# Optimization experiments

Hardware: AMD Instinct MI355X
Metric: run time of the kernel (lower is better)

Reference implementation:

```python
import jax, jax.numpy as jnp
import numpy as np

E = 256
CH = 16  # channel rows; features viewed as (16,16)


def _sigmoid_np(x):
    return 1.0 / (1.0 + np.exp(-x))


def _schedule(emb, comp_l, comp_r, cb, seqs):
    """Phase 1 (host/numpy, mirrors the detached torch control flow):
    runs the iterative argmax-merge tree construction and records the
    integer merge schedule (new composed node pairs per iteration) and the
    (target, ctx_left, ctx_right) prediction triples. Matches Banyan.compose."""
    emb = np.asarray(emb, np.float32)
    sl = _sigmoid_np(np.asarray(comp_l, np.float32))
    sr = _sigmoid_np(np.asarray(comp_r, np.float32))
    cbn = np.asarray(cb, np.float32)
    seqs = np.asarray(seqs, np.int64)

    uniq = np.unique(seqs)
    lookup = np.zeros(uniq.max() + 1, np.int64)
    lookup[uniq] = np.arange(len(uniq))
    lookup[uniq[-1]] = -1  # max unique value acts as pad sentinel (lookup[-1] = -1)
    index = lookup[seqs].copy()
    tokens = uniq[:-1]

    nodes = emb[tokens]  # detached node features used only for similarity / schedule

    def comp(f):  # f: (K,2,16,16)
        return (f[:, 0] * sl + f[:, 1] * sr + cbn).reshape(f.shape[0], -1)

    pair_src = np.zeros((0, 2), np.int64)
    pair_dst = np.zeros((0,), np.int64)
    new_pairs, targets = [], []
    B, W = index.shape

    while W != 1:
        valid = index != -1
        f = nodes[np.clip(index, 0, None)]              # (B,W,E)
        a, b = f[:, :-1], f[:, 1:]
        na = np.linalg.norm(a, axis=-1)
        nb = np.linalg.norm(b, axis=-1)
        cos = (a * b).sum(-1) / np.maximum(na * nb, 1e-8)
        cos = np.where(valid[:, 1:], cos, -np.inf)       # right slot padded -> -inf
        ms_all = np.argmax(cos, axis=1)
        active = ~np.all(index[:, 1:] == -1, axis=1)
        rows = np.nonzero(active)[0]
        ms = ms_all[rows]
        lp, rp = ms, ms + 1
        src = np.stack([index[rows, lp], index[rows, rp]], 1)  # (A,2)

        # dedup against existing composed pairs, then unique new pairs (sorted)
        if pair_src.shape[0] > 0 and src.shape[0] > 0:
            exists = (src[:, None, :] == pair_src[None]).all(-1).any(1)
            newp = src[~exists]
        else:
            newp = src
        if newp.shape[0] > 0:
            newp = np.unique(newp, axis=0)
        base = nodes.shape[0]
        if newp.shape[0] > 0:
            nodes = np.concatenate([nodes, comp(nodes[newp].reshape(-1, 2, CH, CH))], 0)
            pair_src = np.concatenate([pair_src, newp], 0)
            pair_dst = np.concatenate([pair_dst, base + np.arange(newp.shape[0])], 0)
        new_pairs.append(newp.astype(np.int64))

        # neighbourhood targets (get_neighbours): l_t block then r_t block
        lefts, rights = src[:, 0], src[:, 1]
        ls = index[rows, lp - 1].copy()
        ls[lp - 1 == -1] = -1
        rs = index[rows, np.minimum(rp + 1, W - 1)].copy()
        rs[rp + 1 == W] = -2
        targets.append(np.stack([lefts, ls, rights], 1))
        targets.append(np.stack([rights, lefts, rs], 1))

        # point both merged slots at the (possibly shared) composed node id
        if src.shape[0] > 0:
            eq = (src[:, None, :] == pair_src[None]).all(-1)
            nid = pair_dst[eq.argmax(1)]
            index[rows, lp] = nid
            index[rows, rp] = nid

        # reduce frontier: active rows drop the left merge slot, inactive drop last col
        keep = np.ones_like(index, dtype=bool)
        keep[rows, ms] = False
        keep[~active, -1] = False
        index = index[keep].reshape(B, W - 1)
        W -= 1

    targets = np.concatenate(targets, 0).astype(np.int64)
    return tokens, new_pairs, targets


def _replay(emb, comp_l, comp_r, cb, sos, eos, tokens, new_pairs, targets):
    """Phase 2 (jax, differentiable): rebuild node features following the
    recorded schedule, then compute the context->target cross entropy."""
    sl = jax.nn.sigmoid(comp_l)
    sr = jax.nn.sigmoid(comp_r)
    feats = emb[tokens]                                    # (n_tok, E)
    for p in new_pairs:
        if p.shape[0] == 0:
            continue
        f = feats[p].reshape(-1, 2, CH, CH)                # (K,2,16,16)
        feats = jnp.concatenate([feats, (f[:, 0] * sl + f[:, 1] * sr + cb).reshape(-1, E)], 0)
    feats = jnp.concatenate([feats, eos[None, :], sos[None, :]], 0)
    N = feats.shape[0]
    t = np.where(targets < 0, targets + N, targets)        # wrap -1 -> sos, -2 -> eos
    l = feats[t[:, 1]].reshape(-1, CH, CH)
    r = feats[t[:, 2]].reshape(-1, CH, CH)
    outs = (l * sl + r * sr + cb).reshape(-1, E)           # (T,E)
    logits = outs @ feats.T                                # (T,N)
    logp = jax.nn.log_softmax(logits, axis=-1)
    return -jnp.mean(logp[jnp.arange(t.shape[0]), t[:, 0]])


def setup_inputs() -> dict:
    key = jax.random.key(0)
    k1, k2, k3, k4, k5, k6, k7 = jax.random.split(key, 7)
    V, B, L = 30000, 64, 64
    tok = jax.random.randint(k1, (B, L), 0, V - 1, dtype=jnp.int32)
    lengths = jax.random.randint(k2, (B,), L // 2, L + 1, dtype=jnp.int32)
    lengths = lengths.at[0].set(L // 2)  # guarantee pad token (V-1) is present
    x = jnp.where(jnp.arange(L)[None, :] < lengths[:, None], tok, V - 1)
    return {
        "x": x,
        "emb": jax.random.normal(k3, (V, E), jnp.float32),
        "comp_l": jax.random.uniform(k4, (CH,), jnp.float32, 0.6, 0.9),
        "comp_r": jax.random.uniform(k5, (CH,), jnp.float32, 0.6, 0.9),
        "cb": jnp.zeros((CH,), jnp.float32),
        "sos": 0.02 * jax.random.normal(k6, (E,), jnp.float32),
        "eos": 0.02 * jax.random.normal(k7, (E,), jnp.float32),
    }


def reference(x, emb, comp_l, comp_r, cb, sos, eos):
    tokens, new_pairs, targets = _schedule(emb, comp_l, comp_r, cb, x)
    return _replay(emb, comp_l, comp_r, cb, sos, eos, tokens, new_pairs, targets)
```

## Files before the change

### kernel.cpp

```cpp
#include <hip/hip_runtime.h>
#include <math.h>


#define NMAX 8192
#define PRES 30720
#define HBITS 13
#define HSIZE 8192
#define HMASK 8191
#define LOG2E 1.44269504f
#define LN2 0.69314718f

typedef float f32x4 __attribute__((ext_vector_type(4)));
typedef short short8 __attribute__((ext_vector_type(8)));

__device__ __forceinline__ unsigned hash0(int key) {
    return (((unsigned)key) * 2654435761u) >> (32 - HBITS);
}

__device__ __forceinline__ unsigned short f2bf(float f) {
    unsigned u = __float_as_uint(f);
    unsigned r = ((u >> 16) & 1u) + 0x7FFFu;
    return (unsigned short)((u + r) >> 16);
}

__device__ __forceinline__ float rdl_f(float v, int lane) {
    return __int_as_float(__builtin_amdgcn_readlane(__float_as_int(v), lane));
}

#define SUM_STEP(CTRL, X) \
    X += __int_as_float(__builtin_amdgcn_update_dpp(0, __float_as_int(X), CTRL, 0xF, 0xF, true));
#define SUM3_REDUCE(A, B, C) {                                                  \
    SUM_STEP(0x121, A) SUM_STEP(0x121, B) SUM_STEP(0x121, C)                    \
    SUM_STEP(0x122, A) SUM_STEP(0x122, B) SUM_STEP(0x122, C)                    \
    SUM_STEP(0x124, A) SUM_STEP(0x124, B) SUM_STEP(0x124, C)                    \
    SUM_STEP(0x128, A) SUM_STEP(0x128, B) SUM_STEP(0x128, C)                    \
    A = rdl_f(A, 0) + rdl_f(A, 16) + rdl_f(A, 32) + rdl_f(A, 48);               \
    B = rdl_f(B, 0) + rdl_f(B, 16) + rdl_f(B, 32) + rdl_f(B, 48);               \
    C = rdl_f(C, 0) + rdl_f(C, 16) + rdl_f(C, 32) + rdl_f(C, 48);               \
}
#define ARGMAX_STEP(CTRL, V, I) {                                               \
    float _ov = __int_as_float(__builtin_amdgcn_update_dpp(0, __float_as_int(V), CTRL, 0xF, 0xF, true)); \
    int _oi = __builtin_amdgcn_update_dpp(0, I, CTRL, 0xF, 0xF, true);          \
    if (_ov > V || (_ov == V && _oi < I)) { V = _ov; I = _oi; }                 \
}
#define ARGMAX_REDUCE(V, I) {                                                   \
    ARGMAX_STEP(0x121, V, I) ARGMAX_STEP(0x122, V, I)                           \
    ARGMAX_STEP(0x124, V, I) ARGMAX_STEP(0x128, V, I)                           \
    float _v0 = rdl_f(V, 0), _v1 = rdl_f(V, 16), _v2 = rdl_f(V, 32), _v3 = rdl_f(V, 48); \
    int _i0 = __builtin_amdgcn_readlane(I, 0), _i1 = __builtin_amdgcn_readlane(I, 16);   \
    int _i2 = __builtin_amdgcn_readlane(I, 32), _i3 = __builtin_amdgcn_readlane(I, 48);  \
    V = _v0; I = _i0;                                                           \
    if (_v1 > V || (_v1 == V && _i1 < I)) { V = _v1; I = _i1; }                 \
    if (_v2 > V || (_v2 == V && _i2 < I)) { V = _v2; I = _i2; }                 \
    if (_v3 > V || (_v3 == V && _i3 < I)) { V = _v3; I = _i3; }                 \
}

__global__ __launch_bounds__(1024) void prep_kernel(
    const int* __restrict__ x, int* __restrict__ tokens,
    int* __restrict__ meta, int* __restrict__ index_g) {
    __shared__ int pres[PRES];
    __shared__ int part[1024];
    int tid = threadIdx.x;
    for (int i = tid; i < PRES; i += 1024) pres[i] = 0;
    __syncthreads();
    for (int i = tid; i < 4096; i += 1024) pres[x[i]] = 1;
    __syncthreads();
    int base = tid * 30;
    int loc[30];
    int s = 0;
#pragma unroll
    for (int i = 0; i < 30; ++i) { loc[i] = s; s += pres[base + i]; }
    part[tid] = s;
    __syncthreads();
    for (int off = 1; off < 1024; off <<= 1) {
        int v = (tid >= off) ? part[tid - off] : 0;
        __syncthreads();
        part[tid] += v;
        __syncthreads();
    }
    int excl = (tid == 0) ? 0 : part[tid - 1];
    int total = part[1023];
#pragma unroll
    for (int i = 0; i < 30; ++i) {
        if (pres[base + i]) tokens[excl + loc[i]] = base + i;
    }
    if (tid == 0) { meta[0] = total; meta[1] = total - 1; }
    __syncthreads();
#pragma unroll
    for (int i = 0; i < 30; ++i) pres[base + i] = excl + loc[i];
    __syncthreads();
    for (int i = tid; i < 4096; i += 1024) {
        int r = pres[x[i]];
        index_g[i] = (r == total - 1) ? -1 : r;
    }
}

__global__ void copy_feats_kernel(const float* __restrict__ emb, const int* __restrict__ tokens,
                                  const int* __restrict__ meta, float* __restrict__ feats,
                                  float* __restrict__ norms) {
    int n = blockIdx.x;
    if (n >= meta[1]) return;
    int t = tokens[n];
    int k = threadIdx.x;
    const float4* src = (const float4*)(emb + (size_t)t * 256);
    float4* dst = (float4*)(feats + (size_t)n * 256);
    float4 v = src[k];
    dst[k] = v;
    float ss = v.x * v.x + v.y * v.y + v.z * v.z + v.w * v.w;
#pragma unroll
    for (int off = 32; off >= 1; off >>= 1) ss += __shfl_down(ss, off);
    if (k == 0) norms[n] = sqrtf(ss);
}

__global__ void init_cos_kernel(const float* __restrict__ feats, const float* __restrict__ norms,
                                const int* __restrict__ index_g, float* __restrict__ cos_g) {
    int bid = blockIdx.x;
    int b = bid / 63, j = bid % 63;
    int l = index_g[b * 64 + j], r = index_g[b * 64 + j + 1];
    float c = -INFINITY;
    if (r != -1) {
        int k = threadIdx.x;
        const float4* fa = (const float4*)(feats + (size_t)l * 256);
        const float4* fb = (const float4*)(feats + (size_t)r * 256);
        float4 a = fa[k], bb = fb[k];
        float d = a.x * bb.x + a.y * bb.y + a.z * bb.z + a.w * bb.w;
#pragma unroll
        for (int off = 32; off >= 1; off >>= 1) d += __shfl_down(d, off);
        c = d / fmaxf(norms[l] * norms[r], 1e-8f);
    }
    if (threadIdx.x == 0) cos_g[b * 64 + j] = c;
}


__global__ __launch_bounds__(64) void treebuild_kernel(
    const float* __restrict__ feats, const float* __restrict__ norms_g,
    const int* __restrict__ index_g, const float* __restrict__ cos_g,
    float* __restrict__ rowfeats, int4* __restrict__ rec,
    const float* __restrict__ comp_l, const float* __restrict__ comp_r,
    const float* __restrict__ cb) {
    __shared__ float lf[127][256];
    __shared__ int4 s_rec[63];
    int b = blockIdx.x;
    int lane = threadIdx.x;
    int c0 = 4 * (lane & 3);
    float4 sl4 = make_float4(1.f / (1.f + __expf(-comp_l[c0])),
                             1.f / (1.f + __expf(-comp_l[c0 + 1])),
                             1.f / (1.f + __expf(-comp_l[c0 + 2])),
                             1.f / (1.f + __expf(-comp_l[c0 + 3])));
    float4 sr4 = make_float4(1.f / (1.f + __expf(-comp_r[c0])),
                             1.f / (1.f + __expf(-comp_r[c0 + 1])),
                             1.f / (1.f + __expf(-comp_r[c0 + 2])),
                             1.f / (1.f + __expf(-comp_r[c0 + 3])));
    float4 cb4 = make_float4(cb[c0], cb[c0 + 1], cb[c0 + 2], cb[c0 + 3]);

    int gid = index_g[b * 64 + lane];
    int isreal = (gid >= 0) ? 1 : 0;
    for (int j = 0; j < 64; ++j) {
        int g = index_g[b * 64 + j];
        int gc = g < 0 ? 0 : g;
        ((float4*)&lf[j][0])[lane] = ((const float4*)(feats + (size_t)gc * 256))[lane];
    }
    float n0 = (gid >= 0) ? norms_g[gid] : 0.f;
    float n1 = 0.f;
    float cosr = (lane < 63) ? cos_g[b * 64 + lane] : -INFINITY;
    int locid = lane;
    unsigned long long alive = ~0ull;
    int nreal = 64 - __popcll(__ballot(gid < 0));

    float Mv = cosr; int Mi = lane;
    ARGMAX_REDUCE(Mv, Mi);

    for (int it = 0; it < 63; ++it) {
        int act = (nreal >= 2) ? 1 : 0;
        int p = Mi;
        unsigned long long after = (alive >> 1) >> p;
        int q = (p + 1 + __builtin_ctzll(after | 0x8000000000000000ull)) & 63;
        unsigned long long bel = alive & ((1ull << p) - 1ull);
        int pp = bel ? (63 - __builtin_clzll(bel)) : -1;
        unsigned long long aft2 = (q < 63) ? (alive >> (q + 1)) : 0ull;
        int ssp = aft2 ? (q + 1 + __builtin_ctzll(aft2)) : -1;
        int l_loc = __builtin_amdgcn_readlane(locid, p);
        int r_loc = __builtin_amdgcn_readlane(locid, q);
        int lsl = __builtin_amdgcn_readlane(locid, pp < 0 ? 0 : pp);
        int rsl = __builtin_amdgcn_readlane(locid, ssp < 0 ? 0 : ssp);
        int ls_loc = (pp >= 0) ? lsl : -1;
        int rs_loc = (ssp >= 0) ? rsl : -2;
        int Creal = (ssp >= 0) ? __builtin_amdgcn_readlane(isreal, ssp) : 0;
        if (lane == 0)
            s_rec[it] = make_int4(act ? l_loc : -9, r_loc, ls_loc, rs_loc);
        if (act) {
            float4 a = ((const float4*)&lf[l_loc][0])[lane];
            float4 bb = ((const float4*)&lf[r_loc][0])[lane];
            float4 av = (pp >= 0) ? ((const float4*)&lf[ls_loc < 0 ? 0 : ls_loc][0])[lane]
                                  : make_float4(0.f, 0.f, 0.f, 0.f);
            float4 cv = Creal ? ((const float4*)&lf[rs_loc < 0 ? 0 : rs_loc][0])[lane]
                              : make_float4(0.f, 0.f, 0.f, 0.f);
            float mv = (lane == p || lane == q || lane == pp) ? -INFINITY : cosr;
            float Mv2 = mv; int Mi2 = lane;
            ARGMAX_REDUCE(Mv2, Mi2);
            int nl = 64 + it;
            float4 v;
            v.x = a.x * sl4.x + bb.x * sr4.x + cb4.x;
            v.y = a.y * sl4.y + bb.y * sr4.y + cb4.y;
            v.z = a.z * sl4.z + bb.z * sr4.z + cb4.z;
            v.w = a.w * sl4.w + bb.w * sr4.w + cb4.w;
            ((float4*)&lf[nl][0])[lane] = v;
            float sv = v.x * v.x + v.y * v.y + v.z * v.z + v.w * v.w;
            float da = av.x * v.x + av.y * v.y + av.z * v.z + av.w * v.w;
            float dc = cv.x * v.x + cv.y * v.y + cv.z * v.z + cv.w * v.w;
            SUM3_REDUCE(sv, da, dc);
            float nn = sqrtf(sv);
            if (lane == it) n1 = nn;
            float nA = 1.f, nC = 1.f;
            if (pp >= 0) nA = (ls_loc < 64) ? rdl_f(n0, ls_loc) : rdl_f(n1, ls_loc - 64);
            if (Creal)   nC = (rs_loc < 64) ? rdl_f(n0, rs_loc) : rdl_f(n1, rs_loc - 64);
            float cosA = da * __builtin_amdgcn_rcpf(fmaxf(nA * nn, 1e-8f));
            float cosC = Creal ? (dc * __builtin_amdgcn_rcpf(fmaxf(nn * nC, 1e-8f))) : -INFINITY;
            if (lane == p) { cosr = cosC; locid = nl; }
            if (lane == pp) cosr = cosA;
            if (lane == q) cosr = -INFINITY;
            if (pp >= 0 && (cosA > Mv2 || (cosA == Mv2 && pp < Mi2))) { Mv2 = cosA; Mi2 = pp; }
            if (cosC > Mv2 || (cosC == Mv2 && p < Mi2)) { Mv2 = cosC; Mi2 = p; }
            Mv = Mv2; Mi = Mi2;
            alive &= ~(1ull << q);
            nreal -= 1;
        }
    }
    for (int it = 0; it < 63; ++it) {
        ((float4*)(rowfeats + ((size_t)b * 63 + it) * 256))[lane] =
            ((const float4*)&lf[64 + it][0])[lane];
    }
    if (lane < 63) rec[b * 63 + lane] = s_rec[lane];
}


__global__ __launch_bounds__(64) void idassign_kernel(
    const int4* __restrict__ rec, const int* __restrict__ index_g,
    int* __restrict__ targets, int* __restrict__ meta, int* __restrict__ newsrc) {
    __shared__ int s_map[64][128];
    __shared__ int s_hk[HSIZE], s_hv[HSIZE];
    int b = threadIdx.x;
    for (int i = b; i < HSIZE; i += 64) s_hk[i] = -1;
    for (int i = b; i < 4096; i += 64) s_map[i >> 6][i & 63] = index_g[i];
    int N0 = meta[1];
    int Ncur = N0, Tcur = 0;
    __syncthreads();
    int4 R = rec[b * 63];
    for (int it = 0; it < 63; ++it) {
        int4 Rn = R;
        if (it + 1 < 63) Rn = rec[b * 63 + it + 1];
        int act = (R.x != -9) ? 1 : 0;
        int l_g = 0, r_g = 0, key = 0, nid = 0;
        int ls_g = -1, rs_g = -2;
        unsigned h = 0;
        int won = 0, need = 0;
        if (act) {
            l_g = s_map[b][R.x];
            r_g = s_map[b][R.y];
            ls_g = (R.z >= 0) ? s_map[b][R.z] : R.z;
            rs_g = (R.w >= 0) ? s_map[b][R.w] : R.w;
            key = (l_g << HBITS) | r_g;
            h = hash0(key);
            need = 1;
        }
        while (__any(need)) {
            if (need) {
                int prev = atomicCAS(&s_hk[h], -1, key);
                if (prev == -1) { won = 1; need = 0; }
                else if (prev == key) { need = 0; }
                else { h = (h + 1) & HMASK; }
            }
        }
        unsigned long long actmask = __ballot(act != 0);
        unsigned long long winmask = __ballot(won != 0);
        unsigned long long below = (1ull << b) - 1ull;
        int ar = __popcll(actmask & below);
        int nact = __popcll(actmask);
        int newc = __popcll(winmask);
        if (won) {
            nid = Ncur + __popcll(winmask & below);
            s_hv[h] = nid;
        }
        __syncthreads();
        if (act && !won) nid = s_hv[h];
        if (won) newsrc[nid - N0] = (b << 6) | it;
        if (act) {
            int o1 = Tcur + ar;
            targets[o1 * 3 + 0] = l_g;
            targets[o1 * 3 + 1] = ls_g;
            targets[o1 * 3 + 2] = r_g;
            int o2 = Tcur + nact + ar;
            targets[o2 * 3 + 0] = r_g;
            targets[o2 * 3 + 1] = l_g;
            targets[o2 * 3 + 2] = rs_g;
            s_map[b][64 + it] = nid;
        }
        Ncur += newc;
        Tcur += 2 * nact;
        R = Rn;
    }
    if (b == 0) { meta[2] = Ncur; meta[3] = Tcur; meta[4] = Ncur - N0; }
}


__global__ __launch_bounds__(64) void materialize_kernel(
    const float* __restrict__ rowfeats, const int* __restrict__ newsrc,
    const int* __restrict__ meta, float* __restrict__ feats,
    const float* __restrict__ eos, const float* __restrict__ sos) {
    int g = blockIdx.x;
    int lane = threadIdx.x;
    if (g == 4032) {
        int n = meta[2];
        ((float4*)(feats + (size_t)n * 256))[lane] = ((const float4*)eos)[lane];
        ((float4*)(feats + (size_t)(n + 1) * 256))[lane] = ((const float4*)sos)[lane];
        return;
    }
    if (g >= meta[4]) return;
    int pk = newsrc[g];
    int b = pk >> 6, it = pk & 63;
    int N0 = meta[1];
    ((float4*)(feats + (size_t)(N0 + g) * 256))[lane] =
        ((const float4*)(rowfeats + ((size_t)b * 63 + it) * 256))[lane];
}

__global__ __launch_bounds__(256) void convert_feats_kernel(
    const float* __restrict__ feats, short8* __restrict__ fhT) {
    int g = blockIdx.x * 256 + threadIdx.x;
    int tile = g >> 9, rem = g & 511;
    int ks = rem >> 6, lane64 = rem & 63;
    int kq = lane64 >> 4, col = lane64 & 15;
    int row = tile * 16 + col;
    int e0 = (ks * 4 + kq) * 8;
    const float4* src = (const float4*)(feats + (size_t)row * 256 + e0);
    float4 v0 = src[0], v1 = src[1];
    short8 o;
    o[0] = (short)f2bf(v0.x); o[1] = (short)f2bf(v0.y);
    o[2] = (short)f2bf(v0.z); o[3] = (short)f2bf(v0.w);
    o[4] = (short)f2bf(v1.x); o[5] = (short)f2bf(v1.y);
    o[6] = (short)f2bf(v1.z); o[7] = (short)f2bf(v1.w);
    fhT[g] = o;
}

__global__ __launch_bounds__(256) void prep_outs_kernel(
    const float* __restrict__ feats, const int* __restrict__ targets,
    const int* __restrict__ meta, const float* __restrict__ comp_l,
    const float* __restrict__ comp_r, const float* __restrict__ cb,
    unsigned short* __restrict__ oh, float* __restrict__ tdot) {
    int T = meta[3];
    int Ntot = meta[2] + 2;
    int t = blockIdx.x * 4 + (threadIdx.x >> 6);
    if (t >= T) return;
    int lane = threadIdx.x & 63;
    int c0 = 4 * (lane & 3);
    float4 sl4 = make_float4(1.f / (1.f + __expf(-comp_l[c0])),
                             1.f / (1.f + __expf(-comp_l[c0 + 1])),
                             1.f / (1.f + __expf(-comp_l[c0 + 2])),
                             1.f / (1.f + __expf(-comp_l[c0 + 3])));
    float4 sr4 = make_float4(1.f / (1.f + __expf(-comp_r[c0])),
                             1.f / (1.f + __expf(-comp_r[c0 + 1])),
                             1.f / (1.f + __expf(-comp_r[c0 + 2])),
                             1.f / (1.f + __expf(-comp_r[c0 + 3])));
    float4 cb4 = make_float4(cb[c0], cb[c0 + 1], cb[c0 + 2], cb[c0 + 3]);
    int t0 = targets[t * 3 + 0];
    int i1 = targets[t * 3 + 1], i2 = targets[t * 3 + 2];
    if (i1 < 0) i1 += Ntot;
    if (i2 < 0) i2 += Ntot;
    float4 a = ((const float4*)(feats + (size_t)i1 * 256))[lane];
    float4 b = ((const float4*)(feats + (size_t)i2 * 256))[lane];
    float4 ft = ((const float4*)(feats + (size_t)t0 * 256))[lane];
    float4 v;
    v.x = a.x * sl4.x + b.x * sr4.x + cb4.x;
    v.y = a.y * sl4.y + b.y * sr4.y + cb4.y;
    v.z = a.z * sl4.z + b.z * sr4.z + cb4.z;
    v.w = a.w * sl4.w + b.w * sr4.w + cb4.w;
    float d = v.x * ft.x + v.y * ft.y + v.z * ft.z + v.w * ft.w;
#pragma unroll
    for (int off = 32; off >= 1; off >>= 1) d += __shfl_down(d, off);
    if (lane == 0) tdot[t] = d;
    ushort4 h;
    h.x = f2bf(v.x); h.y = f2bf(v.y); h.z = f2bf(v.z); h.w = f2bf(v.w);
    ((ushort4*)(oh + (size_t)t * 256))[lane] = h;
}

__global__ __launch_bounds__(512) void loss_mfma_kernel(
    const short8* __restrict__ fhT, const unsigned short* __restrict__ oh,
    const int* __restrict__ meta, float2* __restrict__ partial) {
    __shared__ float s_m[64][2], s_s[64][2];
    int T = meta[3];
    int Ntot = meta[2] + 2;
    int row0 = blockIdx.x * 64;
    if (row0 >= T) return;
    int slab = blockIdx.y;
    int P = (Ntot + 127) >> 7;
    int cstart = slab * (P << 5);
    int cend = min(Ntot, cstart + (P << 5));
    int tid = threadIdx.x, lane = tid & 63, w = tid >> 6;
    int mq = w >> 1, nq = w & 1;
    int mrow = row0 + mq * 16 + (lane & 15);
    int kq = lane >> 4;
    const short8* pah = (const short8*)(oh + (size_t)mrow * 256);
    short8 Ah[8];
#pragma unroll
    for (int ks = 0; ks < 8; ++ks) Ah[ks] = pah[ks * 4 + kq];
    float m0 = -1e30f, m1 = -1e30f, m2 = -1e30f, m3 = -1e30f;
    float s0 = 0.f, s1 = 0.f, s2 = 0.f, s3 = 0.f;
    for (int nb = cstart; nb < cend; nb += 32) {
        const short8* pb = fhT + ((size_t)(nb >> 4) + nq) * 512;
        f32x4 a0 = {0.f, 0.f, 0.f, 0.f}, a1 = a0;
#pragma unroll
        for (int ks = 0; ks < 4; ++ks) {
            a0 = __builtin_amdgcn_mfma_f32_16x16x32_bf16(Ah[ks], pb[ks * 64 + lane], a0, 0, 0, 0);
            a1 = __builtin_amdgcn_mfma_f32_16x16x32_bf16(Ah[ks + 4], pb[(ks + 4) * 64 + lane], a1, 0, 0, 0);
        }
        int col = nb + nq * 16 + (lane & 15);
        bool cv = col < cend;
        float v0 = cv ? (a0[0] + a1[0]) * LOG2E : -INFINITY;
        float v1 = cv ? (a0[1] + a1[1]) * LOG2E : -INFINITY;
        float v2 = cv ? (a0[2] + a1[2]) * LOG2E : -INFINITY;
        float v3 = cv ? (a0[3] + a1[3]) * LOG2E : -INFINITY;
        if (v0 > m0) { s0 = s0 * exp2f(m0 - v0) + 1.f; m0 = v0; } else s0 += exp2f(v0 - m0);
        if (v1 > m1) { s1 = s1 * exp2f(m1 - v1) + 1.f; m1 = v1; } else s1 += exp2f(v1 - m1);
        if (v2 > m2) { s2 = s2 * exp2f(m2 - v2) + 1.f; m2 = v2; } else s2 += exp2f(v2 - m2);
        if (v3 > m3) { s3 = s3 * exp2f(m3 - v3) + 1.f; m3 = v3; } else s3 += exp2f(v3 - m3);
    }
#pragma unroll
    for (int off = 1; off < 16; off <<= 1) {
        float mo, so, mn;
        mo = __shfl_xor(m0, off); so = __shfl_xor(s0, off);
        mn = fmaxf(m0, mo); s0 = s0 * exp2f(m0 - mn) + so * exp2f(mo - mn); m0 = mn;
        mo = __shfl_xor(m1, off); so = __shfl_xor(s1, off);
        mn = fmaxf(m1, mo); s1 = s1 * exp2f(m1 - mn) + so * exp2f(mo - mn); m1 = mn;
        mo = __shfl_xor(m2, off); so = __shfl_xor(s2, off);
        mn = fmaxf(m2, mo); s2 = s2 * exp2f(m2 - mn) + so * exp2f(mo - mn); m2 = mn;
        mo = __shfl_xor(m3, off); so = __shfl_xor(s3, off);
        mn = fmaxf(m3, mo); s3 = s3 * exp2f(m3 - mn) + so * exp2f(mo - mn); m3 = mn;
    }
    if ((lane & 15) == 0) {
        int rbase = mq * 16 + kq * 4;
        s_m[rbase + 0][nq] = m0; s_s[rbase + 0][nq] = s0;
        s_m[rbase + 1][nq] = m1; s_s[rbase + 1][nq] = s1;
        s_m[rbase + 2][nq] = m2; s_s[rbase + 2][nq] = s2;
        s_m[rbase + 3][nq] = m3; s_s[rbase + 3][nq] = s3;
    }
    __syncthreads();
    if (tid < 64) {
        float ma = s_m[tid][0], mb = s_m[tid][1];
        float mn = fmaxf(ma, mb);
        float ss = s_s[tid][0] * exp2f(ma - mn) + s_s[tid][1] * exp2f(mb - mn);
        partial[(size_t)slab * NMAX + row0 + tid] = make_float2(mn, ss);
    }
}

__global__ __launch_bounds__(1024) void combine_kernel(
    const float2* __restrict__ partial, const float* __restrict__ tdot,
    const int* __restrict__ meta, float* __restrict__ out) {
    __shared__ float red[16];
    int T = meta[3];
    float loss = 0.f;
    for (int r = threadIdx.x; r < T; r += 1024) {
        float2 p0 = partial[r];
        float2 p1 = partial[NMAX + r];
        float2 p2 = partial[2 * NMAX + r];
        float2 p3 = partial[3 * NMAX + r];
        float mn = fmaxf(fmaxf(p0.x, p1.x), fmaxf(p2.x, p3.x));
        float ss = p0.y * exp2f(p0.x - mn) + p1.y * exp2f(p1.x - mn) +
                   p2.y * exp2f(p2.x - mn) + p3.y * exp2f(p3.x - mn);
        loss += (mn + __log2f(ss)) * LN2 - tdot[r];
    }
#pragma unroll
    for (int off = 32; off >= 1; off >>= 1) loss += __shfl_down(loss, off);
    if ((threadIdx.x & 63) == 0) red[threadIdx.x >> 6] = loss;
    __syncthreads();
    if (threadIdx.x < 16) {
        loss = red[threadIdx.x];
#pragma unroll
        for (int off = 8; off >= 1; off >>= 1) loss += __shfl_down(loss, off);
        if (threadIdx.x == 0) out[0] = loss / (float)T;
    }
}

extern "C" void kernel_launch(void* const* d_in, const int* in_sizes, int n_in,
                              void* d_out, int out_size, void* d_ws, size_t ws_size,
                              hipStream_t stream) {
    const int* x = (const int*)d_in[0];
    const float* emb = (const float*)d_in[1];
    const float* comp_l = (const float*)d_in[2];
    const float* comp_r = (const float*)d_in[3];
    const float* cb = (const float*)d_in[4];
    const float* sos = (const float*)d_in[5];
    const float* eos = (const float*)d_in[6];
    float* out = (float*)d_out;

    float* feats = (float*)d_ws;
    float* norms = feats + (size_t)NMAX * 256;
    int* index_g = (int*)(norms + NMAX);
    float* cos_g = (float*)(index_g + 4096);
    int* tokens = (int*)(cos_g + 4096);
    int* targets = tokens + 4096;
    int* meta = targets + NMAX * 3;
    float* tdot = (float*)(meta + 64);
    float2* partial = (float2*)(tdot + NMAX);
    int4* rec = (int4*)(partial + 4 * NMAX);
    int* newsrc = (int*)(rec + 64 * 63);
    float* rowfeats = (float*)(newsrc + 4096);
    short8* fhT = (short8*)(rowfeats + (size_t)64 * 63 * 256);
    unsigned short* oh = (unsigned short*)(fhT + (size_t)NMAX * 32);

    prep_kernel<<<1, 1024, 0, stream>>>(x, tokens, meta, index_g);
    copy_feats_kernel<<<4096, 64, 0, stream>>>(emb, tokens, meta, feats, norms);
    init_cos_kernel<<<64 * 63, 64, 0, stream>>>(feats, norms, index_g, cos_g);
    treebuild_kernel<<<64, 64, 0, stream>>>(feats, norms, index_g, cos_g,
                                            rowfeats, rec, comp_l, comp_r, cb);
    idassign_kernel<<<1, 64, 0, stream>>>(rec, index_g, targets, meta, newsrc);
    materialize_kernel<<<4033, 64, 0, stream>>>(rowfeats, newsrc, meta, feats, eos, sos);
    convert_feats_kernel<<<1024, 256, 0, stream>>>(feats, fhT);
    prep_outs_kernel<<<2016, 256, 0, stream>>>(feats, targets, meta, comp_l, comp_r,
                                               cb, oh, tdot);
    loss_mfma_kernel<<<dim3(126, 4), 512, 0, stream>>>(fhT, oh, meta, partial);
    combine_kernel<<<1, 1024, 0, stream>>>(partial, tdot, meta, out);
}
```

Before: 214.1 us.

## Split treebuild across two wavefronts and widen loss vocab slabs to eight

The treebuild kernel now runs two wavefronts per block. One computes the composed node and its three dot-product reductions while the other runs the argmax reduction, and the results are exchanged through double-buffered shared memory with a block barrier each iteration. The loss MFMA kernel splits the vocabulary into eight column slabs instead of four, giving more blocks, and the combine kernel merges eight partial log-sum-exp pairs. This trades a per-iteration __syncthreads on the serial critical path, plus more partial traffic, for overlapping the two reductions and better occupancy in the loss GEMM.

After: 212.0 us. About the same (-1.0%).

```diff
diff --git a/kernel.cpp b/kernel.cpp
--- a/kernel.cpp
+++ b/kernel.cpp
@@ -9,6 +9,7 @@
 #define HMASK 8191
 #define LOG2E 1.44269504f
 #define LN2 0.69314718f
+#define NSLAB 8
 
 typedef float f32x4 __attribute__((ext_vector_type(4)));
 typedef short short8 __attribute__((ext_vector_type(8)));
@@ -132,7 +133,7 @@
 }
 
 
-__global__ __launch_bounds__(64) void treebuild_kernel(
+__global__ __launch_bounds__(128) void treebuild_kernel(
     const float* __restrict__ feats, const float* __restrict__ norms_g,
     const int* __restrict__ index_g, const float* __restrict__ cos_g,
     float* __restrict__ rowfeats, int4* __restrict__ rec,
@@ -140,8 +141,11 @@
     const float* __restrict__ cb) {
     __shared__ float lf[127][256];
     __shared__ int4 s_rec[63];
+    __shared__ float s_sv[2], s_da[2], s_dc[2], s_mv[2];
+    __shared__ int s_mi[2];
     int b = blockIdx.x;
-    int lane = threadIdx.x;
+    int tid = threadIdx.x;
+    int lane = tid & 63, wv = tid >> 6;
     int c0 = 4 * (lane & 3);
     float4 sl4 = make_float4(1.f / (1.f + __expf(-comp_l[c0])),
                              1.f / (1.f + __expf(-comp_l[c0 + 1])),
@@ -155,7 +159,7 @@
 
     int gid = index_g[b * 64 + lane];
     int isreal = (gid >= 0) ? 1 : 0;
-    for (int j = 0; j < 64; ++j) {
+    for (int j = wv * 32; j < wv * 32 + 32; ++j) {
         int g = index_g[b * 64 + j];
         int gc = g < 0 ? 0 : g;
         ((float4*)&lf[j][0])[lane] = ((const float4*)(feats + (size_t)gc * 256))[lane];
@@ -166,6 +170,7 @@
     int locid = lane;
     unsigned long long alive = ~0ull;
     int nreal = 64 - __popcll(__ballot(gid < 0));
+    __syncthreads();
 
     float Mv = cosr; int Mi = lane;
     ARGMAX_REDUCE(Mv, Mi);
@@ -186,29 +191,38 @@
         int ls_loc = (pp >= 0) ? lsl : -1;
         int rs_loc = (ssp >= 0) ? rsl : -2;
         int Creal = (ssp >= 0) ? __builtin_amdgcn_readlane(isreal, ssp) : 0;
-        if (lane == 0)
+        if (wv == 0 && lane == 0)
             s_rec[it] = make_int4(act ? l_loc : -9, r_loc, ls_loc, rs_loc);
         if (act) {
-            float4 a = ((const float4*)&lf[l_loc][0])[lane];
-            float4 bb = ((const float4*)&lf[r_loc][0])[lane];
-            float4 av = (pp >= 0) ? ((const float4*)&lf[ls_loc < 0 ? 0 : ls_loc][0])[lane]
+            int par = it & 1;
+            int nl = 64 + it;
+            if (wv == 1) {
+                float4 a = ((const float4*)&lf[l_loc][0])[lane];
+                float4 bb = ((const float4*)&lf[r_loc][0])[lane];
+                float4 av = (pp >= 0) ? ((const float4*)&lf[ls_loc < 0 ? 0 : ls_loc][0])[lane]
+                                      : make_float4(0.f, 0.f, 0.f, 0.f);
+                float4 cv = Creal ? ((const float4*)&lf[rs_loc < 0 ? 0 : rs_loc][0])[lane]
                                   : make_float4(0.f, 0.f, 0.f, 0.f);
-            float4 cv = Creal ? ((const float4*)&lf[rs_loc < 0 ? 0 : rs_loc][0])[lane]
-                              : make_float4(0.f, 0.f, 0.f, 0.f);
-            float mv = (lane == p || lane == q || lane == pp) ? -INFINITY : cosr;
-            float Mv2 = mv; int Mi2 = lane;
-            ARGMAX_REDUCE(Mv2, Mi2);
-            int nl = 64 + it;
-            float4 v;
-            v.x = a.x * sl4.x + bb.x * sr4.x + cb4.x;
-            v.y = a.y * sl4.y + bb.y * sr4.y + cb4.y;
-            v.z = a.z * sl4.z + bb.z * sr4.z + cb4.z;
-            v.w = a.w * sl4.w + bb.w * sr4.w + cb4.w;
-            ((float4*)&lf[nl][0])[lane] = v;
-            float sv = v.x * v.x + v.y * v.y + v.z * v.z + v.w * v.w;
-            float da = av.x * v.x + av.y * v.y + av.z * v.z + av.w * v.w;
-            float dc = cv.x * v.x + cv.y * v.y + cv.z * v.z + cv.w * v.w;
-            SUM3_REDUCE(sv, da, dc);
+                float4 v;
+                v.x = a.x * sl4.x + bb.x * sr4.x + cb4.x;
+                v.y = a.y * sl4.y + bb.y * sr4.y + cb4.y;
+                v.z = a.z * sl4.z + bb.z * sr4.z + cb4.z;
+                v.w = a.w * sl4.w + bb.w * sr4.w + cb4.w;
+                ((float4*)&lf[nl][0])[lane] = v;
+                float sv = v.x * v.x + v.y * v.y + v.z * v.z + v.w * v.w;
+                float da = av.x * v.x + av.y * v.y + av.z * v.z + av.w * v.w;
+                float dc = cv.x * v.x + cv.y * v.y + cv.z * v.z + cv.w * v.w;
+                SUM3_REDUCE(sv, da, dc);
+                if (lane == 0) { s_sv[par] = sv; s_da[par] = da; s_dc[par] = dc; }
+            } else {
+                float mv = (lane == p || lane == q || lane == pp) ? -INFINITY : cosr;
+                float Mv2 = mv; int Mi2 = lane;
+                ARGMAX_REDUCE(Mv2, Mi2);
+                if (lane == 0) { s_mv[par] = Mv2; s_mi[par] = Mi2; }
+            }
+            __syncthreads();
+            float sv = s_sv[par], da = s_da[par], dc = s_dc[par];
+            float Mv2 = s_mv[par]; int Mi2 = s_mi[par];
             float nn = sqrtf(sv);
             if (lane == it) n1 = nn;
             float nA = 1.f, nC = 1.f;
@@ -226,11 +240,12 @@
             nreal -= 1;
         }
     }
-    for (int it = 0; it < 63; ++it) {
+    __syncthreads();
+    for (int it = wv; it < 63; it += 2) {
         ((float4*)(rowfeats + ((size_t)b * 63 + it) * 256))[lane] =
             ((const float4*)&lf[64 + it][0])[lane];
     }
-    if (lane < 63) rec[b * 63 + lane] = s_rec[lane];
+    if (wv == 0 && lane < 63) rec[b * 63 + lane] = s_rec[lane];
 }
 
 
@@ -391,7 +406,7 @@
     int row0 = blockIdx.x * 64;
     if (row0 >= T) return;
     int slab = blockIdx.y;
-    int P = (Ntot + 127) >> 7;
+    int P = (Ntot + 32 * NSLAB - 1) / (32 * NSLAB);
     int cstart = slab * (P << 5);
     int cend = min(Ntot, cstart + (P << 5));
     int tid = threadIdx.x, lane = tid & 63, w = tid >> 6;
@@ -458,13 +473,16 @@
     int T = meta[3];
     float loss = 0.f;
     for (int r = threadIdx.x; r < T; r += 1024) {
-        float2 p0 = partial[r];
-        float2 p1 = partial[NMAX + r];
-        float2 p2 = partial[2 * NMAX + r];
-        float2 p3 = partial[3 * NMAX + r];
-        float mn = fmaxf(fmaxf(p0.x, p1.x), fmaxf(p2.x, p3.x));
-        float ss = p0.y * exp2f(p0.x - mn) + p1.y * exp2f(p1.x - mn) +
-                   p2.y * exp2f(p2.x - mn) + p3.y * exp2f(p3.x - mn);
+        float2 ps[NSLAB];
+        float mn = -1e30f;
+#pragma unroll
+        for (int s = 0; s < NSLAB; ++s) {
+            ps[s] = partial[(size_t)s * NMAX + r];
+            mn = fmaxf(mn, ps[s].x);
+        }
+        float ss = 0.f;
+#pragma unroll
+        for (int s = 0; s < NSLAB; ++s) ss += ps[s].y * exp2f(ps[s].x - mn);
         loss += (mn + __log2f(ss)) * LN2 - tdot[r];
     }
 #pragma unroll
@@ -500,7 +518,7 @@
     int* meta = targets + NMAX * 3;
     float* tdot = (float*)(meta + 64);
     float2* partial = (float2*)(tdot + NMAX);
-    int4* rec = (int4*)(partial + 4 * NMAX);
+    int4* rec = (int4*)(partial + NSLAB * NMAX);
     int* newsrc = (int*)(rec + 64 * 63);
     float* rowfeats = (float*)(newsrc + 4096);
     short8* fhT = (short8*)(rowfeats + (size_t)64 * 63 * 256);
@@ -509,13 +527,13 @@
     prep_kernel<<<1, 1024, 0, stream>>>(x, tokens, meta, index_g);
     copy_feats_kernel<<<4096, 64, 0, stream>>>(emb, tokens, meta, feats, norms);
     init_cos_kernel<<<64 * 63, 64, 0, stream>>>(feats, norms, index_g, cos_g);
-    treebuild_kernel<<<64, 64, 0, stream>>>(feats, norms, index_g, cos_g,
-                                            rowfeats, rec, comp_l, comp_r, cb);
+    treebuild_kernel<<<64, 128, 0, stream>>>(feats, norms, index_g, cos_g,
+                                             rowfeats, rec, comp_l, comp_r, cb);
     idassign_kernel<<<1, 64, 0, stream>>>(rec, index_g, targets, meta, newsrc);
     materialize_kernel<<<4033, 64, 0, stream>>>(rowfeats, newsrc, meta, feats, eos, sos);
     convert_feats_kernel<<<1024, 256, 0, stream>>>(feats, fhT);
     prep_outs_kernel<<<2016, 256, 0, stream>>>(feats, targets, meta, comp_l, comp_r,
                                                cb, oh, tdot);
-    loss_mfma_kernel<<<dim3(126, 4), 512, 0, stream>>>(fhT, oh, meta, partial);
+    loss_mfma_kernel<<<dim3(126, NSLAB), 512, 0, stream>>>(fhT, oh, meta, partial);
     combine_kernel<<<1, 1024, 0, stream>>>(partial, tdot, meta, out);
 }
```

## Fuse setup kernels, widen loss column split, use lazy online-softmax rescale

Applied to the files above, without the earlier changes.

Merges the embedding copy and initial cosine kernels into one launch. The cosine path now reads directly from emb through tokens and computes its own norms, which removes the dependency between the two. Also merges the bf16 feature conversion with output preparation, and folds the LOG2E scale into the bf16 outputs. Doubles the loss kernel's column slabs from 4 to 8 to raise parallelism, and replaces the per-element max update with a lazy rescale that triggers only when the new value exceeds the running max by 32 in log2 space. This trades fewer launches and less exp/branch work for more partial results to combine and a small bf16 rounding change from pre-scaling.

Result: faster. 206.1 us (-3.8%).

```diff
diff --git a/kernel.cpp b/kernel.cpp
--- a/kernel.cpp
+++ b/kernel.cpp
@@ -9,6 +9,7 @@
 #define HMASK 8191
 #define LOG2E 1.44269504f
 #define LN2 0.69314718f
+#define NSLAB 8
 
 typedef float f32x4 __attribute__((ext_vector_type(4)));
 typedef short short8 __attribute__((ext_vector_type(8)));
@@ -95,40 +96,45 @@
     }
 }
 
-__global__ void copy_feats_kernel(const float* __restrict__ emb, const int* __restrict__ tokens,
-                                  const int* __restrict__ meta, float* __restrict__ feats,
-                                  float* __restrict__ norms) {
-    int n = blockIdx.x;
-    if (n >= meta[1]) return;
-    int t = tokens[n];
+__global__ __launch_bounds__(64) void prefeats_kernel(
+    const float* __restrict__ emb, const int* __restrict__ tokens,
+    const int* __restrict__ meta, const int* __restrict__ index_g,
+    float* __restrict__ feats, float* __restrict__ norms,
+    float* __restrict__ cos_g) {
+    int g = blockIdx.x;
     int k = threadIdx.x;
-    const float4* src = (const float4*)(emb + (size_t)t * 256);
-    float4* dst = (float4*)(feats + (size_t)n * 256);
-    float4 v = src[k];
-    dst[k] = v;
-    float ss = v.x * v.x + v.y * v.y + v.z * v.z + v.w * v.w;
-#pragma unroll
-    for (int off = 32; off >= 1; off >>= 1) ss += __shfl_down(ss, off);
-    if (k == 0) norms[n] = sqrtf(ss);
-}
-
-__global__ void init_cos_kernel(const float* __restrict__ feats, const float* __restrict__ norms,
-                                const int* __restrict__ index_g, float* __restrict__ cos_g) {
-    int bid = blockIdx.x;
-    int b = bid / 63, j = bid % 63;
+    if (g < 4096) {
+        int n = g;
+        if (n >= meta[1]) return;
+        int t = tokens[n];
+        float4 v = ((const float4*)(emb + (size_t)t * 256))[k];
+        ((float4*)(feats + (size_t)n * 256))[k] = v;
+        float ss = v.x * v.x + v.y * v.y + v.z * v.z + v.w * v.w;
+#pragma unroll
+        for (int off = 32; off >= 1; off >>= 1) ss += __shfl_down(ss, off);
+        if (k == 0) norms[n] = sqrtf(ss);
+        return;
+    }
+    int idx = g - 4096;
+    int b = idx / 63, j = idx % 63;
     int l = index_g[b * 64 + j], r = index_g[b * 64 + j + 1];
     float c = -INFINITY;
     if (r != -1) {
-        int k = threadIdx.x;
-        const float4* fa = (const float4*)(feats + (size_t)l * 256);
-        const float4* fb = (const float4*)(feats + (size_t)r * 256);
-        float4 a = fa[k], bb = fb[k];
+        int tl = tokens[l], tr = tokens[r];
+        float4 a = ((const float4*)(emb + (size_t)tl * 256))[k];
+        float4 bb = ((const float4*)(emb + (size_t)tr * 256))[k];
         float d = a.x * bb.x + a.y * bb.y + a.z * bb.z + a.w * bb.w;
-#pragma unroll
-        for (int off = 32; off >= 1; off >>= 1) d += __shfl_down(d, off);
-        c = d / fmaxf(norms[l] * norms[r], 1e-8f);
-    }
-    if (threadIdx.x == 0) cos_g[b * 64 + j] = c;
+        float na = a.x * a.x + a.y * a.y + a.z * a.z + a.w * a.w;
+        float nb = bb.x * bb.x + bb.y * bb.y + bb.z * bb.z + bb.w * bb.w;
+#pragma unroll
+        for (int off = 32; off >= 1; off >>= 1) {
+            d += __shfl_down(d, off);
+            na += __shfl_down(na, off);
+            nb += __shfl_down(nb, off);
+        }
+        c = d / fmaxf(sqrtf(na) * sqrtf(nb), 1e-8f);
+    }
+    if (k == 0) cos_g[b * 64 + j] = c;
 }
 
 
@@ -323,32 +329,32 @@
         ((const float4*)(rowfeats + ((size_t)b * 63 + it) * 256))[lane];
 }
 
-__global__ __launch_bounds__(256) void convert_feats_kernel(
-    const float* __restrict__ feats, short8* __restrict__ fhT) {
-    int g = blockIdx.x * 256 + threadIdx.x;
-    int tile = g >> 9, rem = g & 511;
-    int ks = rem >> 6, lane64 = rem & 63;
-    int kq = lane64 >> 4, col = lane64 & 15;
-    int row = tile * 16 + col;
-    int e0 = (ks * 4 + kq) * 8;
-    const float4* src = (const float4*)(feats + (size_t)row * 256 + e0);
-    float4 v0 = src[0], v1 = src[1];
-    short8 o;
-    o[0] = (short)f2bf(v0.x); o[1] = (short)f2bf(v0.y);
-    o[2] = (short)f2bf(v0.z); o[3] = (short)f2bf(v0.w);
-    o[4] = (short)f2bf(v1.x); o[5] = (short)f2bf(v1.y);
-    o[6] = (short)f2bf(v1.z); o[7] = (short)f2bf(v1.w);
-    fhT[g] = o;
-}
-
-__global__ __launch_bounds__(256) void prep_outs_kernel(
+__global__ __launch_bounds__(256) void convout_kernel(
     const float* __restrict__ feats, const int* __restrict__ targets,
     const int* __restrict__ meta, const float* __restrict__ comp_l,
     const float* __restrict__ comp_r, const float* __restrict__ cb,
-    unsigned short* __restrict__ oh, float* __restrict__ tdot) {
+    short8* __restrict__ fhT, unsigned short* __restrict__ oh,
+    float* __restrict__ tdot) {
+    if (blockIdx.x < 1024) {
+        int g = blockIdx.x * 256 + threadIdx.x;
+        int tile = g >> 9, rem = g & 511;
+        int ks = rem >> 6, lane64 = rem & 63;
+        int kq = lane64 >> 4, col = lane64 & 15;
+        int row = tile * 16 + col;
+        int e0 = (ks * 4 + kq) * 8;
+        const float4* src = (const float4*)(feats + (size_t)row * 256 + e0);
+        float4 v0 = src[0], v1 = src[1];
+        short8 o;
+        o[0] = (short)f2bf(v0.x); o[1] = (short)f2bf(v0.y);
+        o[2] = (short)f2bf(v0.z); o[3] = (short)f2bf(v0.w);
+        o[4] = (short)f2bf(v1.x); o[5] = (short)f2bf(v1.y);
+        o[6] = (short)f2bf(v1.z); o[7] = (short)f2bf(v1.w);
+        fhT[g] = o;
+        return;
+    }
     int T = meta[3];
     int Ntot = meta[2] + 2;
-    int t = blockIdx.x * 4 + (threadIdx.x >> 6);
+    int t = (blockIdx.x - 1024) * 4 + (threadIdx.x >> 6);
     if (t >= T) return;
     int lane = threadIdx.x & 63;
     int c0 = 4 * (lane & 3);
@@ -378,7 +384,8 @@
     for (int off = 32; off >= 1; off >>= 1) d += __shfl_down(d, off);
     if (lane == 0) tdot[t] = d;
     ushort4 h;
-    h.x = f2bf(v.x); h.y = f2bf(v.y); h.z = f2bf(v.z); h.w = f2bf(v.w);
+    h.x = f2bf(v.x * LOG2E); h.y = f2bf(v.y * LOG2E);
+    h.z = f2bf(v.z * LOG2E); h.w = f2bf(v.w * LOG2E);
     ((ushort4*)(oh + (size_t)t * 256))[lane] = h;
 }
 
@@ -391,7 +398,7 @@
     int row0 = blockIdx.x * 64;
     if (row0 >= T) return;
     int slab = blockIdx.y;
-    int P = (Ntot + 127) >> 7;
+    int P = (Ntot + 32 * NSLAB - 1) / (32 * NSLAB);
     int cstart = slab * (P << 5);
     int cend = min(Ntot, cstart + (P << 5));
     int tid = threadIdx.x, lane = tid & 63, w = tid >> 6;
@@ -414,14 +421,15 @@
         }
         int col = nb + nq * 16 + (lane & 15);
         bool cv = col < cend;
-        float v0 = cv ? (a0[0] + a1[0]) * LOG2E : -INFINITY;
-        float v1 = cv ? (a0[1] + a1[1]) * LOG2E : -INFINITY;
-        float v2 = cv ? (a0[2] + a1[2]) * LOG2E : -INFINITY;
-        float v3 = cv ? (a0[3] + a1[3]) * LOG2E : -INFINITY;
-        if (v0 > m0) { s0 = s0 * exp2f(m0 - v0) + 1.f; m0 = v0; } else s0 += exp2f(v0 - m0);
-        if (v1 > m1) { s1 = s1 * exp2f(m1 - v1) + 1.f; m1 = v1; } else s1 += exp2f(v1 - m1);
-        if (v2 > m2) { s2 = s2 * exp2f(m2 - v2) + 1.f; m2 = v2; } else s2 += exp2f(v2 - m2);
-        if (v3 > m3) { s3 = s3 * exp2f(m3 - v3) + 1.f; m3 = v3; } else s3 += exp2f(v3 - m3);
+        float v0 = cv ? (a0[0] + a1[0]) : -INFINITY;
+        float v1 = cv ? (a0[1] + a1[1]) : -INFINITY;
+        float v2 = cv ? (a0[2] + a1[2]) : -INFINITY;
+        float v3 = cv ? (a0[3] + a1[3]) : -INFINITY;
+        float d0 = v0 - m0, d1 = v1 - m1, d2 = v2 - m2, d3 = v3 - m3;
+        if (d0 > 32.f) { s0 = s0 * exp2f(-d0) + 1.f; m0 = v0; } else s0 += exp2f(d0);
+        if (d1 > 32.f) { s1 = s1 * exp2f(-d1) + 1.f; m1 = v1; } else s1 += exp2f(d1);
+        if (d2 > 32.f) { s2 = s2 * exp2f(-d2) + 1.f; m2 = v2; } else s2 += exp2f(d2);
+        if (d3 > 32.f) { s3 = s3 * exp2f(-d3) + 1.f; m3 = v3; } else s3 += exp2f(d3);
     }
 #pragma unroll
     for (int off = 1; off < 16; off <<= 1) {
@@ -458,13 +466,16 @@
     int T = meta[3];
     float loss = 0.f;
     for (int r = threadIdx.x; r < T; r += 1024) {
-        float2 p0 = partial[r];
-        float2 p1 = partial[NMAX + r];
-        float2 p2 = partial[2 * NMAX + r];
-        float2 p3 = partial[3 * NMAX + r];
-        float mn = fmaxf(fmaxf(p0.x, p1.x), fmaxf(p2.x, p3.x));
-        float ss = p0.y * exp2f(p0.x - mn) + p1.y * exp2f(p1.x - mn) +
-                   p2.y * exp2f(p2.x - mn) + p3.y * exp2f(p3.x - mn);
+        float2 ps[NSLAB];
+        float mn = -1e30f;
+#pragma unroll
+        for (int s = 0; s < NSLAB; ++s) {
+            ps[s] = partial[(size_t)s * NMAX + r];
+            mn = fmaxf(mn, ps[s].x);
+        }
+        float ss = 0.f;
+#pragma unroll
+        for (int s = 0; s < NSLAB; ++s) ss += ps[s].y * exp2f(ps[s].x - mn);
         loss += (mn + __log2f(ss)) * LN2 - tdot[r];
     }
 #pragma unroll
@@ -500,22 +511,21 @@
     int* meta = targets + NMAX * 3;
     float* tdot = (float*)(meta + 64);
     float2* partial = (float2*)(tdot + NMAX);
-    int4* rec = (int4*)(partial + 4 * NMAX);
+    int4* rec = (int4*)(partial + NSLAB * NMAX);
     int* newsrc = (int*)(rec + 64 * 63);
     float* rowfeats = (float*)(newsrc + 4096);
     short8* fhT = (short8*)(rowfeats + (size_t)64 * 63 * 256);
     unsigned short* oh = (unsigned short*)(fhT + (size_t)NMAX * 32);
 
     prep_kernel<<<1, 1024, 0, stream>>>(x, tokens, meta, index_g);
-    copy_feats_kernel<<<4096, 64, 0, stream>>>(emb, tokens, meta, feats, norms);
-    init_cos_kernel<<<64 * 63, 64, 0, stream>>>(feats, norms, index_g, cos_g);
+    prefeats_kernel<<<8128, 64, 0, stream>>>(emb, tokens, meta, index_g,
+                                             feats, norms, cos_g);
     treebuild_kernel<<<64, 64, 0, stream>>>(feats, norms, index_g, cos_g,
                                             rowfeats, rec, comp_l, comp_r, cb);
     idassign_kernel<<<1, 64, 0, stream>>>(rec, index_g, targets, meta, newsrc);
     materialize_kernel<<<4033, 64, 0, stream>>>(rowfeats, newsrc, meta, feats, eos, sos);
-    convert_feats_kernel<<<1024, 256, 0, stream>>>(feats, fhT);
-    prep_outs_kernel<<<2016, 256, 0, stream>>>(feats, targets, meta, comp_l, comp_r,
-                                               cb, oh, tdot);
-    loss_mfma_kernel<<<dim3(126, 4), 512, 0, stream>>>(fhT, oh, meta, partial);
+    convout_kernel<<<3040, 256, 0, stream>>>(feats, targets, meta, comp_l, comp_r,
+                                             cb, fhT, oh, tdot);
+    loss_mfma_kernel<<<dim3(126, NSLAB), 512, 0, stream>>>(fhT, oh, meta, partial);
     combine_kernel<<<1, 1024, 0, stream>>>(partial, tdot, meta, out);
 }
```
